# Kernel optimization log

Hardware: AMD Instinct MI355X
Metric: run time of the kernel (lower is better)

Reference implementation:

```python
import jax, jax.numpy as jnp
import numpy as np

NUM_HEADS = 16
HEAD_DIM = 96          # dim=1536 / 16 heads
ROPE_HALF = HEAD_DIM // 2   # 48 rotary frequencies
FREQ_PER_AXIS = ROPE_HALF // 3  # 16 frequencies per 3D coordinate axis
ROPE_BASE = 10000.0


def _rope_sincos(coords):
    # coords: [B, T, 3] -> sin, cos: [B, T, ROPE_HALF]
    inv_freq = 1.0 / (ROPE_BASE ** (jnp.arange(FREQ_PER_AXIS, dtype=jnp.float32) / FREQ_PER_AXIS))
    # angles per axis: [B, T, 3, F] -> concat axes -> [B, T, 3*F]
    ang = coords[..., :, None] * inv_freq  # [B, T, 3, F]
    ang = ang.reshape(*coords.shape[:-1], ROPE_HALF)
    return jnp.sin(ang), jnp.cos(ang)


def _apply_rotary(x, sin, cos):
    # x: [B, H, T, D]; sin/cos: [B, T, D/2] broadcast over heads
    s = sin[:, None, :, :]
    c = cos[:, None, :, :]
    x1, x2 = x[..., :ROPE_HALF], x[..., ROPE_HALF:]
    return jnp.concatenate([x1 * c - x2 * s, x2 * c + x1 * s], axis=-1)


def setup_inputs() -> dict:
    key = jax.random.key(0)
    ks = jax.random.split(key, 8)
    B, Tq, Tk, D = 2, 1024, 2048, 1536
    std = 1.0 / np.sqrt(D)
    return {
        "x": jax.random.normal(ks[0], (B, Tq, D), jnp.float32),
        "memory": jax.random.normal(ks[1], (B, Tk, D), jnp.float32),
        "query_coords": jax.random.normal(ks[2], (B, Tq, 3), jnp.float32),
        "memory_coords": jax.random.normal(ks[3], (B, Tk, 3), jnp.float32),
        "Wq": jax.random.normal(ks[4], (D, D), jnp.float32) * std,
        "bq": jnp.zeros((D,), jnp.float32),
        "Wk": jax.random.normal(ks[5], (D, D), jnp.float32) * std,
        "bk": jnp.zeros((D,), jnp.float32),
        "Wv": jax.random.normal(ks[6], (D, D), jnp.float32) * std,
        "bv": jnp.zeros((D,), jnp.float32),
        "Wo": jax.random.normal(ks[7], (D, D), jnp.float32) * std,
        "bo": jnp.zeros((D,), jnp.float32),
    }


def reference(x, memory, query_coords, memory_coords, Wq, bq, Wk, bk, Wv, bv, Wo, bo):
    B, Tq, D = x.shape
    Tk = memory.shape[1]
    H, Hd = NUM_HEADS, HEAD_DIM

    # projections (nn.Linear: y = x @ W^T + b)
    q = (jnp.einsum('btd,ed->bte', x, Wq) + bq).reshape(B, Tq, H, Hd).transpose(0, 2, 1, 3)
    k = (jnp.einsum('btd,ed->bte', memory, Wk) + bk).reshape(B, Tk, H, Hd).transpose(0, 2, 1, 3)
    v = (jnp.einsum('btd,ed->bte', memory, Wv) + bv).reshape(B, Tk, H, Hd).transpose(0, 2, 1, 3)

    # 3D-coordinate RoPE (identity augmentation: shift=0, jitter=1, rescale=1)
    q_sin, q_cos = _rope_sincos(query_coords)
    k_sin, k_cos = _rope_sincos(memory_coords)
    q = _apply_rotary(q, q_sin, q_cos)
    k = _apply_rotary(k, k_sin, k_cos)

    # SDPA (standard scaling): softmax(q k^T / sqrt(Hd)) v
    scale = 1.0 / jnp.sqrt(jnp.asarray(Hd, jnp.float32))
    scores = jnp.einsum('bhqd,bhkd->bhqk', q, k) * scale
    attn = jax.nn.softmax(scores, axis=-1)
    out = jnp.einsum('bhqk,bhkd->bhqd', attn, v)  # [B, H, Tq, Hd]

    out = out.transpose(0, 2, 1, 3).reshape(B, Tq, D)
    return jnp.einsum('btd,ed->bte', out, Wo) + bo
```

## Files before the change

### kernel.cpp

```cpp
#include <hip/hip_runtime.h>
#include <math.h>

typedef _Float16 f16;
typedef __attribute__((ext_vector_type(4))) _Float16 f16x4;
typedef __attribute__((ext_vector_type(8))) _Float16 f16x8;
typedef __attribute__((ext_vector_type(4))) float f32x4;
typedef __attribute__((ext_vector_type(16))) float f32x16;

#define NB 2
#define NH 16
#define TQ 1024
#define TK 2048
#define DM 1536
#define HD 96
#define RH 48

__device__ __forceinline__ f32x4 mfma16(f16x8 a, f16x8 b, f32x4 c) {
    return __builtin_amdgcn_mfma_f32_16x16x32_f16(a, b, c, 0, 0, 0);
}

#define GLDS16(gptr, lptr) __builtin_amdgcn_global_load_lds( \
    (const __attribute__((address_space(1))) unsigned int*)(gptr), \
    (__attribute__((address_space(3))) unsigned int*)(lptr), 16, 0, 0)

__global__ void cvt6(const float4* __restrict__ Wq, const float4* __restrict__ Wk,
                     const float4* __restrict__ Wv, const float4* __restrict__ Wo,
                     const float4* __restrict__ X,  const float4* __restrict__ M,
                     f16x4* __restrict__ oq, f16x4* __restrict__ ok,
                     f16x4* __restrict__ ov, f16x4* __restrict__ oo,
                     f16x4* __restrict__ ox, f16x4* __restrict__ om,
                     int nw4, int nx4, int nm4) {
    int i = blockIdx.x * 256 + threadIdx.x;
    const int y = blockIdx.y;
    const int n = (y < 4) ? nw4 : (y == 4 ? nx4 : nm4);
    if (i >= n) return;
    const float4* in = y == 0 ? Wq : y == 1 ? Wk : y == 2 ? Wv : y == 3 ? Wo : y == 4 ? X : M;
    f16x4* out      = y == 0 ? oq : y == 1 ? ok : y == 2 ? ov : y == 3 ? oo : y == 4 ? ox : om;
    float4 v = in[i];
    f16x4 o;
    o[0] = (f16)v.x; o[1] = (f16)v.y; o[2] = (f16)v.z; o[3] = (f16)v.w;
    out[i] = o;
}

__global__ void rope_tab2(const float* __restrict__ cq, const float* __restrict__ cm,
                          float* __restrict__ sq, float* __restrict__ cqo,
                          float* __restrict__ sk, float* __restrict__ cko,
                          int nq, int nk) {
    int i = blockIdx.x * 256 + threadIdx.x;
    int n = blockIdx.y == 0 ? nq : nk;
    if (i >= n) return;
    const float* coords = blockIdx.y == 0 ? cq : cm;
    float* sinT = blockIdx.y == 0 ? sq : sk;
    float* cosT = blockIdx.y == 0 ? cqo : cko;
    int bt = i / 48, idx = i - bt * 48;
    int axis = idx >> 4, f = idx & 15;
    float inv = powf(10000.f, -(float)f * (1.f / 16.f));
    float ang = coords[bt * 3 + axis] * inv;
    sinT[i] = sinf(ang);
    cosT[i] = cosf(ang);
}

__global__ void ropek4(f16* __restrict__ qk, const float* __restrict__ sinT,
                       const float* __restrict__ cosT, int n) {
    int i = blockIdx.x * 256 + threadIdx.x;
    if (i >= n) return;
    int j = i % 12, row = i / 12;
    int p0 = j * 4;
    int t = row & (TK - 1);
    int b = row / (NH * TK);
    long base = (long)row * 128;
    float4 sv = *(const float4*)&sinT[((long)b * TK + t) * 48 + p0];
    float4 cv = *(const float4*)&cosT[((long)b * TK + t) * 48 + p0];
    f16x4 x1 = *(const f16x4*)&qk[base + p0];
    f16x4 x2 = *(const f16x4*)&qk[base + p0 + RH];
    f16x4 o1, o2;
    float s[4] = {sv.x, sv.y, sv.z, sv.w}, c[4] = {cv.x, cv.y, cv.z, cv.w};
#pragma unroll
    for (int e = 0; e < 4; e++) {
        float a = (float)x1[e], bb = (float)x2[e];
        o1[e] = (f16)(a * c[e] - bb * s[e]);
        o2[e] = (f16)(bb * c[e] + a * s[e]);
    }
    *(f16x4*)&qk[base + p0] = o1;
    *(f16x4*)&qk[base + p0 + RH] = o2;
}

template <int CFG>
__global__ __launch_bounds__(CFG == 0 ? 512 : 256, CFG == 0 ? 1 : 2)
void gemmP(const f16* __restrict__ Aq, const f16* __restrict__ Akv,
           const f16* __restrict__ Wqp, const f16* __restrict__ Wkp, const f16* __restrict__ Wvp,
           const float* __restrict__ bqp, const float* __restrict__ bkp, const float* __restrict__ bvp,
           f16* __restrict__ outq, f16* __restrict__ outk, f16* __restrict__ outv,
           float* __restrict__ outo) {
    constexpr int BMx = CFG == 0 ? 256 : 128;
    constexpr int BNx = CFG == 0 ? 256 : 128;
    constexpr int TPB = CFG == 0 ? 512 : 256;
    constexpr int MI  = CFG == 0 ? 8 : 4;
    constexpr int NI  = 4;
    constexpr int ABUF = BMx * 64;
    constexpr int BUFSZ = (BMx + BNx) * 64;
    constexpr int NT = DM / 64;

    __shared__ f16 Buf[2][BUFSZ];

    const int tid = threadIdx.x, w = tid >> 6, lane = tid & 63;
    const int l15 = lane & 15, g = lane >> 4;

    int sel = 0, mt, nt;
    const f16* A; const f16* W; const float* bias;
    if constexpr (CFG == 0) {
        const int bid = blockIdx.x;
        const int wid = (bid & 7) * 30 + (bid >> 3);
        if (wid < 48)       { sel = 0; mt = wid / 6;        nt = wid - mt * 6;        A = Aq;  W = Wqp; bias = bqp; }
        else if (wid < 144) { sel = 1; int r = wid - 48;  mt = r / 6; nt = r - mt * 6; A = Akv; W = Wkp; bias = bkp; }
        else                { sel = 2; int r = wid - 144; mt = r / 6; nt = r - mt * 6; A = Akv; W = Wvp; bias = bvp; }
    } else {
        const int bid = blockIdx.x;
        const int wid = (bid & 7) * 24 + (bid >> 3);
        mt = wid / 12; nt = wid - mt * 12;
        A = Aq; W = Wqp; bias = bqp;
    }
    const int m0 = mt * BMx, n0 = nt * BNx;
    const int wm = (w & 1) * (MI * 16);
    const int wn = (w >> 1) * 64;

    int src[4];
#pragma unroll
    for (int r = 0; r < 4; r++) {
        int L = r * (TPB * 16) + tid * 16;
        int row = L >> 7, seg = (L >> 4) & 7;
        src[r] = row * DM + ((seg ^ (row & 7)) << 3);
    }
    const f16* Ag = A + (long)m0 * DM;
    const f16* Bg = W + (long)n0 * DM;

    int aoff[MI][2], boff[NI][2];
#pragma unroll
    for (int i = 0; i < MI; i++) {
        int row = wm + i * 16 + l15;
#pragma unroll
        for (int s = 0; s < 2; s++)
            aoff[i][s] = row * 64 + (((s * 4 + g) ^ (row & 7)) << 3);
    }
#pragma unroll
    for (int j = 0; j < NI; j++) {
        int row = wn + j * 16 + l15;
#pragma unroll
        for (int s = 0; s < 2; s++)
            boff[j][s] = ABUF + row * 64 + (((s * 4 + g) ^ (row & 7)) << 3);
    }

#define STG(bufp, kt) do { \
    _Pragma("unroll") for (int r_ = 0; r_ < 4; r_++) { \
        GLDS16(Ag + src[r_] + (kt) * 64, &Buf[bufp][r_ * (TPB * 8) + w * 512]); \
        GLDS16(Bg + src[r_] + (kt) * 64, &Buf[bufp][ABUF + r_ * (TPB * 8) + w * 512]); \
    } \
} while (0)

    f32x4 acc[MI][NI] = {};

#define COMPUTE(bufp) do { \
    f16x8 bf[NI][2]; \
    _Pragma("unroll") for (int j_ = 0; j_ < NI; j_++) \
        _Pragma("unroll") for (int s_ = 0; s_ < 2; s_++) \
            bf[j_][s_] = *(const f16x8*)&Buf[bufp][boff[j_][s_]]; \
    __builtin_amdgcn_s_setprio(1); \
    _Pragma("unroll") for (int i_ = 0; i_ < MI; i_++) { \
        f16x8 a0 = *(const f16x8*)&Buf[bufp][aoff[i_][0]]; \
        f16x8 a1 = *(const f16x8*)&Buf[bufp][aoff[i_][1]]; \
        _Pragma("unroll") for (int j_ = 0; j_ < NI; j_++) { \
            acc[i_][j_] = mfma16(a0, bf[j_][0], acc[i_][j_]); \
            acc[i_][j_] = mfma16(a1, bf[j_][1], acc[i_][j_]); \
        } \
    } \
    __builtin_amdgcn_s_setprio(0); \
} while (0)

    STG(0, 0);
#pragma unroll 1
    for (int t = 0; t < NT; t += 2) {
        STG(1, t + 1);
        asm volatile("s_waitcnt vmcnt(8)" ::: "memory");
        __builtin_amdgcn_s_barrier();
        __builtin_amdgcn_sched_barrier(0);
        COMPUTE(0);
        __builtin_amdgcn_sched_barrier(0);
        __builtin_amdgcn_s_barrier();
        if (t + 2 < NT) {
            STG(0, t + 2);
            asm volatile("s_waitcnt vmcnt(8)" ::: "memory");
        } else {
            asm volatile("s_waitcnt vmcnt(0)" ::: "memory");
        }
        __builtin_amdgcn_s_barrier();
        __builtin_amdgcn_sched_barrier(0);
        COMPUTE(1);
        __builtin_amdgcn_sched_barrier(0);
        __builtin_amdgcn_s_barrier();
    }
#undef STG
#undef COMPUTE

#pragma unroll
    for (int i = 0; i < MI; i++) {
#pragma unroll
        for (int j = 0; j < NI; j++) {
            const int n = n0 + wn + j * 16 + l15;
            const int mb = m0 + wm + i * 16 + g * 4;
            if constexpr (CFG == 1) {
#pragma unroll
                for (int r = 0; r < 4; r++)
                    outo[(long)(mb + r) * DM + n] = acc[i][j][r] + bias[n];
            } else {
                const int hh = n / HD, hd = n - hh * HD;
                if (sel == 0) {
#pragma unroll
                    for (int r = 0; r < 4; r++) {
                        int m = mb + r, bq = m >> 10, t = m & (TQ - 1);
                        outq[(((long)bq * NH + hh) * TQ + t) * 96 + hd] = (f16)(acc[i][j][r] + bias[n]);
                    }
                } else if (sel == 1) {
#pragma unroll
                    for (int r = 0; r < 4; r++) {
                        int m = mb + r, bq = m >> 11, t = m & (TK - 1);
                        outk[(((long)bq * NH + hh) * TK + t) * 128 + hd] = (f16)(acc[i][j][r] + bias[n]);
                    }
                } else {
                    int bq = mb >> 11, t = mb & (TK - 1);
                    f16x4 pk;
#pragma unroll
                    for (int r = 0; r < 4; r++) pk[r] = (f16)(acc[i][j][r] + bias[n]);
                    *(f16x4*)&outv[(((long)bq * NH + hh) * HD + hd) * TK + t] = pk;
                }
            }
        }
    }
}

__global__ __launch_bounds__(256, 2) void attn_fwd(
    const f16* __restrict__ Q, const f16* __restrict__ Kg,
    const f16* __restrict__ Vg, const float* __restrict__ sinq,
    const float* __restrict__ cosq, f16* __restrict__ O) {
    __shared__ f16 Kl[2][64 * 128];
    __shared__ f16 Vl[2][96 * 64];
    __shared__ f16 Pl[4][32 * 64];

    const int tid = threadIdx.x, w = tid >> 6, lane = tid & 63;
    const int q31 = lane & 31, hf = lane >> 5;
    const int half = w >> 1, u = w & 1;

    const int linear = blockIdx.x + (int)(gridDim.x * (blockIdx.y + gridDim.y * blockIdx.z));
    const int wid = (linear & 7) * 64 + (linear >> 3);
    const int qc = wid & 15, h = (wid >> 4) & 15, b = wid >> 8;

    const long kbase = (long)(b * NH + h) * TK * 128;
    const long vbase = (long)(b * NH + h) * HD * TK;
    const long qbase = (long)(b * NH + h) * TQ * 96;
    const int q0 = qc * 64 + u * 32;

    int ksrc[8], vsrc[6];
#pragma unroll
    for (int i = 0; i < 8; i++) {
        int L = (u * 8 + i) * 1024 + lane * 16;
        int r = L >> 8, s = (L >> 4) & 15;
        ksrc[i] = r * 128 + ((s ^ (r & 7)) << 3);
    }
#pragma unroll
    for (int i = 0; i < 6; i++) {
        int L = (u * 6 + i) * 1024 + lane * 16;
        int r = L >> 7, s = (L >> 4) & 7;
        vsrc[i] = r * TK + ((s ^ (r & 7)) << 3);
    }

    f16x8 qf[6];
#pragma unroll
    for (int s = 0; s < 6; s++)
        qf[s] = *(const f16x8*)&Q[qbase + (long)(q0 + q31) * 96 + hf * 8 + 16 * s];
    {
        const float QS = 0.10206207261596577f * 1.4426950408889634f;
        const long tb = ((long)b * TQ + q0 + q31) * 48 + hf * 8;
#pragma unroll
        for (int s = 0; s < 3; s++) {
            float4 s0 = *(const float4*)&sinq[tb + 16 * s];
            float4 s1 = *(const float4*)&sinq[tb + 16 * s + 4];
            float4 c0 = *(const float4*)&cosq[tb + 16 * s];
            float4 c1 = *(const float4*)&cosq[tb + 16 * s + 4];
            float sv[8] = {s0.x, s0.y, s0.z, s0.w, s1.x, s1.y, s1.z, s1.w};
            float cv[8] = {c0.x, c0.y, c0.z, c0.w, c1.x, c1.y, c1.z, c1.w};
#pragma unroll
            for (int e = 0; e < 8; e++) {
                float x1 = (float)qf[s][e], x2 = (float)qf[s + 3][e];
                qf[s][e]     = (f16)((x1 * cv[e] - x2 * sv[e]) * QS);
                qf[s + 3][e] = (f16)((x2 * cv[e] + x1 * sv[e]) * QS);
            }
        }
    }

    float mx = -3e38f, ls = 0.f;
    f32x16 acc[3] = {};

#define STAGE(c_) do { \
    const f16* kp_ = Kg + kbase + (long)(half * 16 + (c_)) * (64 * 128); \
    _Pragma("unroll") for (int i_ = 0; i_ < 8; i_++) \
        GLDS16(kp_ + ksrc[i_], &Kl[half][(u * 8 + i_) * 512]); \
    const f16* vp_ = Vg + vbase + (half * 16 + (c_)) * 64; \
    _Pragma("unroll") for (int i_ = 0; i_ < 6; i_++) \
        GLDS16(vp_ + vsrc[i_], &Vl[half][(u * 6 + i_) * 512]); \
} while (0)

    STAGE(0);

    for (int c = 0; c < 16; ++c) {
        __syncthreads();

        f32x16 st[2] = {};
#pragma unroll
        for (int kt = 0; kt < 2; kt++)
#pragma unroll
            for (int s = 0; s < 6; s++) {
                f16x8 kf = *(const f16x8*)&Kl[half][(kt * 32 + q31) * 128 +
                                                    (((hf + 2 * s) ^ (q31 & 7)) << 3)];
                st[kt] = __builtin_amdgcn_mfma_f32_32x32x16_f16(kf, qf[s], st[kt], 0, 0, 0);
            }

        float t16[16];
#pragma unroll
        for (int r = 0; r < 16; r++) t16[r] = fmaxf(st[0][r], st[1][r]);
#pragma unroll
        for (int o = 8; o >= 1; o >>= 1)
#pragma unroll
            for (int r = 0; r < o; r++) t16[r] = fmaxf(t16[r], t16[r + o]);
        float cm = fmaxf(t16[0], __shfl_xor(t16[0], 32));
        float mn = fmaxf(mx, cm);
        float corr = exp2f(mx - mn);
        mx = mn;
#pragma unroll
        for (int kt = 0; kt < 2; kt++)
#pragma unroll
            for (int r = 0; r < 16; r++) st[kt][r] = exp2f(st[kt][r] - mn);
        float s16[16];
#pragma unroll
        for (int r = 0; r < 16; r++) s16[r] = st[0][r] + st[1][r];
#pragma unroll
        for (int o = 8; o >= 1; o >>= 1)
#pragma unroll
            for (int r = 0; r < o; r++) s16[r] += s16[r + o];
        ls = ls * corr + s16[0];
#pragma unroll
        for (int dt = 0; dt < 3; dt++)
#pragma unroll
            for (int r = 0; r < 16; r++) acc[dt][r] *= corr;

#pragma unroll
        for (int kt = 0; kt < 2; kt++)
#pragma unroll
            for (int jq = 0; jq < 4; jq++) {
                f16x4 pk;
#pragma unroll
                for (int e = 0; e < 4; e++) pk[e] = (f16)st[kt][jq * 4 + e];
                int seg = kt * 4 + jq;
                *(f16x4*)&Pl[w][q31 * 64 + ((seg ^ (q31 & 7)) << 3) + hf * 4] = pk;
            }

#pragma unroll
        for (int ks = 0; ks < 4; ks++) {
            f16x8 pf = *(const f16x8*)&Pl[w][q31 * 64 + (((hf + 2 * ks) ^ (q31 & 7)) << 3)];
#pragma unroll
            for (int dt = 0; dt < 3; dt++) {
                f16x8 vf = *(const f16x8*)&Vl[half][(dt * 32 + q31) * 64 +
                                                    (((hf + 2 * ks) ^ (q31 & 7)) << 3)];
                acc[dt] = __builtin_amdgcn_mfma_f32_32x32x16_f16(vf, pf, acc[dt], 0, 0, 0);
            }
        }

        __syncthreads();
        if (c < 15) STAGE(c + 1);
    }

    ls += __shfl_xor(ls, 32);
    float* dump = (float*)&Kl[0][0] + u * (64 * 52);
    __syncthreads();
    if (half == 1) {
        float* dl = dump + lane * 52;
        dl[0] = mx; dl[1] = ls;
#pragma unroll
        for (int dt = 0; dt < 3; dt++)
#pragma unroll
            for (int r = 0; r < 16; r++) dl[2 + dt * 16 + r] = acc[dt][r];
    }
    __syncthreads();
    if (half == 0) {
        const float* dl = dump + lane * 52;
        float mb = dl[0], lsb = dl[1];
        float mf = fmaxf(mx, mb);
        float ca = exp2f(mx - mf), cb = exp2f(mb - mf);
        float inv = 1.f / (ls * ca + lsb * cb);
        const long orow = (long)(b * TQ + q0 + q31) * DM + h * 96;
#pragma unroll
        for (int dt = 0; dt < 3; dt++)
#pragma unroll
            for (int jq = 0; jq < 4; jq++) {
                f16x4 ov;
#pragma unroll
                for (int e = 0; e < 4; e++) {
                    int r = jq * 4 + e;
                    ov[e] = (f16)((acc[dt][r] * ca + dl[2 + dt * 16 + r] * cb) * inv);
                }
                *(f16x4*)&O[orow + dt * 32 + jq * 8 + hf * 4] = ov;
            }
    }
}

extern "C" void kernel_launch(void* const* d_in, const int* in_sizes, int n_in,
                              void* d_out, int out_size, void* d_ws, size_t ws_size,
                              hipStream_t stream) {
    const float* x   = (const float*)d_in[0];
    const float* mem = (const float*)d_in[1];
    const float* qc  = (const float*)d_in[2];
    const float* mc  = (const float*)d_in[3];
    const float* Wq  = (const float*)d_in[4];
    const float* bq  = (const float*)d_in[5];
    const float* Wk  = (const float*)d_in[6];
    const float* bk  = (const float*)d_in[7];
    const float* Wv  = (const float*)d_in[8];
    const float* bv  = (const float*)d_in[9];
    const float* Wo  = (const float*)d_in[10];
    const float* bo  = (const float*)d_in[11];
    float* out = (float*)d_out;

    const long nx  = (long)NB * TQ * DM;
    const long nm  = (long)NB * TK * DM;
    const long nw  = (long)DM * DM;
    const long nq  = (long)NB * NH * TQ * 96;
    const long nkp = (long)NB * NH * TK * 128;
    const long nvt = (long)NB * NH * HD * TK;

    char* ws = (char*)d_ws;
    size_t off = 0;
    auto alloc = [&](size_t bytes) { size_t o = off; off = (off + bytes + 255) & ~(size_t)255; return o; };
    f16* x16   = (f16*)(ws + alloc(nx * 2));
    f16* mem16 = (f16*)(ws + alloc(nm * 2));
    f16* wq16  = (f16*)(ws + alloc(nw * 2));
    f16* wk16  = (f16*)(ws + alloc(nw * 2));
    f16* wv16  = (f16*)(ws + alloc(nw * 2));
    f16* wo16  = (f16*)(ws + alloc(nw * 2));
    f16* q16   = (f16*)(ws + alloc(nq * 2));
    f16* k16p  = (f16*)(ws + alloc(nkp * 2));
    f16* vt16  = (f16*)(ws + alloc(nvt * 2));
    float* sinq = (float*)(ws + alloc((size_t)NB * TQ * 48 * 4));
    float* cosq = (float*)(ws + alloc((size_t)NB * TQ * 48 * 4));
    float* sink = (float*)(ws + alloc((size_t)NB * TK * 48 * 4));
    float* cosk = (float*)(ws + alloc((size_t)NB * TK * 48 * 4));
    f16* at16 = x16;

    cvt6<<<dim3((int)(nm / 4 / 256), 6), 256, 0, stream>>>(
        (const float4*)Wq, (const float4*)Wk, (const float4*)Wv, (const float4*)Wo,
        (const float4*)x, (const float4*)mem,
        (f16x4*)wq16, (f16x4*)wk16, (f16x4*)wv16, (f16x4*)wo16,
        (f16x4*)x16, (f16x4*)mem16,
        (int)(nw / 4), (int)(nx / 4), (int)(nm / 4));

    rope_tab2<<<dim3((NB * TK * 48 + 255) / 256, 2), 256, 0, stream>>>(
        qc, mc, sinq, cosq, sink, cosk, NB * TQ * 48, NB * TK * 48);

    gemmP<0><<<240, 512, 0, stream>>>(
        x16, mem16, wq16, wk16, wv16, bq, bk, bv, q16, k16p, vt16, nullptr);

    ropek4<<<(NB * NH * TK * 12 + 255) / 256, 256, 0, stream>>>(
        k16p, sink, cosk, NB * NH * TK * 12);

    attn_fwd<<<dim3(16, 16, 2), 256, 0, stream>>>(q16, k16p, vt16, sinq, cosq, at16);

    gemmP<1><<<192, 256, 0, stream>>>(
        at16, nullptr, wo16, nullptr, nullptr, bo, nullptr, nullptr,
        nullptr, nullptr, nullptr, out);
}
```

Before: 155.8 us.

## Load QKV GEMM weight tiles directly into registers instead of LDS

The templated GEMM is split into a dedicated QKV kernel and an output-projection kernel. In the QKV kernel, the B (weight) operand fragments are now loaded from global memory straight into registers, double-buffered, and only the A tile is staged through LDS. This halves LDS usage and LDS read traffic per tile, at the cost of more vector registers and uncoalesced, non-shared global loads of weights across waves. The O-projection kernel keeps the previous scheme.

```diff
diff --git a/kernel.cpp b/kernel.cpp
--- a/kernel.cpp
+++ b/kernel.cpp
@@ -85,43 +85,163 @@
     *(f16x4*)&qk[base + p0 + RH] = o2;
 }
 
-template <int CFG>
-__global__ __launch_bounds__(CFG == 0 ? 512 : 256, CFG == 0 ? 1 : 2)
-void gemmP(const f16* __restrict__ Aq, const f16* __restrict__ Akv,
-           const f16* __restrict__ Wqp, const f16* __restrict__ Wkp, const f16* __restrict__ Wvp,
-           const float* __restrict__ bqp, const float* __restrict__ bkp, const float* __restrict__ bvp,
-           f16* __restrict__ outq, f16* __restrict__ outk, f16* __restrict__ outv,
-           float* __restrict__ outo) {
-    constexpr int BMx = CFG == 0 ? 256 : 128;
-    constexpr int BNx = CFG == 0 ? 256 : 128;
-    constexpr int TPB = CFG == 0 ? 512 : 256;
-    constexpr int MI  = CFG == 0 ? 8 : 4;
-    constexpr int NI  = 4;
-    constexpr int ABUF = BMx * 64;
-    constexpr int BUFSZ = (BMx + BNx) * 64;
+__global__ __launch_bounds__(512, 1)
+void gemmQKV(const f16* __restrict__ Aq, const f16* __restrict__ Akv,
+             const f16* __restrict__ Wqp, const f16* __restrict__ Wkp, const f16* __restrict__ Wvp,
+             const float* __restrict__ bqp, const float* __restrict__ bkp, const float* __restrict__ bvp,
+             f16* __restrict__ outq, f16* __restrict__ outk, f16* __restrict__ outv) {
+    constexpr int MI = 8, NI = 4;
     constexpr int NT = DM / 64;
 
-    __shared__ f16 Buf[2][BUFSZ];
+    __shared__ f16 Buf[2][256 * 64];
 
     const int tid = threadIdx.x, w = tid >> 6, lane = tid & 63;
     const int l15 = lane & 15, g = lane >> 4;
 
     int sel = 0, mt, nt;
     const f16* A; const f16* W; const float* bias;
-    if constexpr (CFG == 0) {
+    {
         const int bid = blockIdx.x;
         const int wid = (bid & 7) * 30 + (bid >> 3);
         if (wid < 48)       { sel = 0; mt = wid / 6;        nt = wid - mt * 6;        A = Aq;  W = Wqp; bias = bqp; }
         else if (wid < 144) { sel = 1; int r = wid - 48;  mt = r / 6; nt = r - mt * 6; A = Akv; W = Wkp; bias = bkp; }
         else                { sel = 2; int r = wid - 144; mt = r / 6; nt = r - mt * 6; A = Akv; W = Wvp; bias = bvp; }
-    } else {
-        const int bid = blockIdx.x;
-        const int wid = (bid & 7) * 24 + (bid >> 3);
-        mt = wid / 12; nt = wid - mt * 12;
-        A = Aq; W = Wqp; bias = bqp;
-    }
-    const int m0 = mt * BMx, n0 = nt * BNx;
-    const int wm = (w & 1) * (MI * 16);
+    }
+    const int m0 = mt * 256, n0 = nt * 256;
+    const int wm = (w & 1) * 128;
+    const int wn = (w >> 1) * 64;
+
+    int src[4];
+#pragma unroll
+    for (int r = 0; r < 4; r++) {
+        int L = r * 8192 + tid * 16;
+        int row = L >> 7, seg = (L >> 4) & 7;
+        src[r] = row * DM + ((seg ^ (row & 7)) << 3);
+    }
+    const f16* Ag = A + (long)m0 * DM;
+
+    int aoff[MI][2];
+#pragma unroll
+    for (int i = 0; i < MI; i++) {
+        int row = wm + i * 16 + l15;
+#pragma unroll
+        for (int s = 0; s < 2; s++)
+            aoff[i][s] = row * 64 + (((s * 4 + g) ^ (row & 7)) << 3);
+    }
+
+    const f16* bptr[NI];
+#pragma unroll
+    for (int j = 0; j < NI; j++)
+        bptr[j] = W + (long)(n0 + wn + j * 16 + l15) * DM + g * 8;
+
+#define STG(bufp, kt) do { \
+    _Pragma("unroll") for (int r_ = 0; r_ < 4; r_++) \
+        GLDS16(Ag + src[r_] + (kt) * 64, &Buf[bufp][r_ * 4096 + w * 512]); \
+} while (0)
+
+#define LDB(breg, kt) do { \
+    _Pragma("unroll") for (int j_ = 0; j_ < NI; j_++) \
+        _Pragma("unroll") for (int s_ = 0; s_ < 2; s_++) \
+            breg[j_][s_] = *(const f16x8*)(bptr[j_] + (kt) * 64 + s_ * 32); \
+} while (0)
+
+    f32x4 acc[MI][NI] = {};
+
+#define COMPUTE(bufp, breg) do { \
+    __builtin_amdgcn_s_setprio(1); \
+    _Pragma("unroll") for (int i_ = 0; i_ < MI; i_++) { \
+        f16x8 a0 = *(const f16x8*)&Buf[bufp][aoff[i_][0]]; \
+        f16x8 a1 = *(const f16x8*)&Buf[bufp][aoff[i_][1]]; \
+        _Pragma("unroll") for (int j_ = 0; j_ < NI; j_++) { \
+            acc[i_][j_] = mfma16(a0, breg[j_][0], acc[i_][j_]); \
+            acc[i_][j_] = mfma16(a1, breg[j_][1], acc[i_][j_]); \
+        } \
+    } \
+    __builtin_amdgcn_s_setprio(0); \
+} while (0)
+
+    f16x8 bA[NI][2], bB[NI][2];
+    STG(0, 0);
+    LDB(bA, 0);
+
+#pragma unroll 1
+    for (int t = 0; t < NT; t += 2) {
+        if (t + 1 < NT) {
+            STG(1, t + 1);
+            LDB(bB, t + 1);
+            asm volatile("s_waitcnt vmcnt(12)" ::: "memory");
+        } else {
+            asm volatile("s_waitcnt vmcnt(0)" ::: "memory");
+        }
+        __builtin_amdgcn_s_barrier();
+        __builtin_amdgcn_sched_barrier(0);
+        COMPUTE(0, bA);
+        __builtin_amdgcn_sched_barrier(0);
+        __builtin_amdgcn_s_barrier();
+        if (t + 2 < NT) {
+            STG(0, t + 2);
+            LDB(bA, t + 2);
+            asm volatile("s_waitcnt vmcnt(12)" ::: "memory");
+        } else {
+            asm volatile("s_waitcnt vmcnt(0)" ::: "memory");
+        }
+        __builtin_amdgcn_s_barrier();
+        __builtin_amdgcn_sched_barrier(0);
+        COMPUTE(1, bB);
+        __builtin_amdgcn_sched_barrier(0);
+        __builtin_amdgcn_s_barrier();
+    }
+#undef STG
+#undef LDB
+#undef COMPUTE
+
+#pragma unroll
+    for (int i = 0; i < MI; i++) {
+#pragma unroll
+        for (int j = 0; j < NI; j++) {
+            const int n = n0 + wn + j * 16 + l15;
+            const int mb = m0 + wm + i * 16 + g * 4;
+            const int hh = n / HD, hd = n - hh * HD;
+            if (sel == 0) {
+#pragma unroll
+                for (int r = 0; r < 4; r++) {
+                    int m = mb + r, bq = m >> 10, t = m & (TQ - 1);
+                    outq[(((long)bq * NH + hh) * TQ + t) * 96 + hd] = (f16)(acc[i][j][r] + bias[n]);
+                }
+            } else if (sel == 1) {
+#pragma unroll
+                for (int r = 0; r < 4; r++) {
+                    int m = mb + r, bq = m >> 11, t = m & (TK - 1);
+                    outk[(((long)bq * NH + hh) * TK + t) * 128 + hd] = (f16)(acc[i][j][r] + bias[n]);
+                }
+            } else {
+                int bq = mb >> 11, t = mb & (TK - 1);
+                f16x4 pk;
+#pragma unroll
+                for (int r = 0; r < 4; r++) pk[r] = (f16)(acc[i][j][r] + bias[n]);
+                *(f16x4*)&outv[(((long)bq * NH + hh) * HD + hd) * TK + t] = pk;
+            }
+        }
+    }
+}
+
+__global__ __launch_bounds__(256, 2)
+void gemmO(const f16* __restrict__ A, const f16* __restrict__ W,
+           const float* __restrict__ bias, float* __restrict__ outo) {
+    constexpr int TPB = 256, MI = 4, NI = 4;
+    constexpr int ABUF = 128 * 64;
+    constexpr int BUFSZ = 256 * 64;
+    constexpr int NT = DM / 64;
+
+    __shared__ f16 Buf[2][BUFSZ];
+
+    const int tid = threadIdx.x, w = tid >> 6, lane = tid & 63;
+    const int l15 = lane & 15, g = lane >> 4;
+    const int bid = blockIdx.x;
+    const int wid = (bid & 7) * 24 + (bid >> 3);
+    const int mt = wid / 12, nt = wid - mt * 12;
+    const int m0 = mt * 128, n0 = nt * 128;
+    const int wm = (w & 1) * 64;
     const int wn = (w >> 1) * 64;
 
     int src[4];
@@ -207,32 +327,9 @@
         for (int j = 0; j < NI; j++) {
             const int n = n0 + wn + j * 16 + l15;
             const int mb = m0 + wm + i * 16 + g * 4;
-            if constexpr (CFG == 1) {
-#pragma unroll
-                for (int r = 0; r < 4; r++)
-                    outo[(long)(mb + r) * DM + n] = acc[i][j][r] + bias[n];
-            } else {
-                const int hh = n / HD, hd = n - hh * HD;
-                if (sel == 0) {
-#pragma unroll
-                    for (int r = 0; r < 4; r++) {
-                        int m = mb + r, bq = m >> 10, t = m & (TQ - 1);
-                        outq[(((long)bq * NH + hh) * TQ + t) * 96 + hd] = (f16)(acc[i][j][r] + bias[n]);
-                    }
-                } else if (sel == 1) {
-#pragma unroll
-                    for (int r = 0; r < 4; r++) {
-                        int m = mb + r, bq = m >> 11, t = m & (TK - 1);
-                        outk[(((long)bq * NH + hh) * TK + t) * 128 + hd] = (f16)(acc[i][j][r] + bias[n]);
-                    }
-                } else {
-                    int bq = mb >> 11, t = mb & (TK - 1);
-                    f16x4 pk;
-#pragma unroll
-                    for (int r = 0; r < 4; r++) pk[r] = (f16)(acc[i][j][r] + bias[n]);
-                    *(f16x4*)&outv[(((long)bq * NH + hh) * HD + hd) * TK + t] = pk;
-                }
-            }
+#pragma unroll
+            for (int r = 0; r < 4; r++)
+                outo[(long)(mb + r) * DM + n] = acc[i][j][r] + bias[n];
         }
     }
 }
@@ -463,15 +560,13 @@
     rope_tab2<<<dim3((NB * TK * 48 + 255) / 256, 2), 256, 0, stream>>>(
         qc, mc, sinq, cosq, sink, cosk, NB * TQ * 48, NB * TK * 48);
 
-    gemmP<0><<<240, 512, 0, stream>>>(
-        x16, mem16, wq16, wk16, wv16, bq, bk, bv, q16, k16p, vt16, nullptr);
+    gemmQKV<<<240, 512, 0, stream>>>(
+        x16, mem16, wq16, wk16, wv16, bq, bk, bv, q16, k16p, vt16);
 
     ropek4<<<(NB * NH * TK * 12 + 255) / 256, 256, 0, stream>>>(
         k16p, sink, cosk, NB * NH * TK * 12);
 
     attn_fwd<<<dim3(16, 16, 2), 256, 0, stream>>>(q16, k16p, vt16, sinq, cosq, at16);
 
-    gemmP<1><<<192, 256, 0, stream>>>(
-        at16, nullptr, wo16, nullptr, nullptr, bo, nullptr, nullptr,
-        nullptr, nullptr, nullptr, out);
-}
+    gemmO<<<192, 256, 0, stream>>>(at16, wo16, bo, out);
+}
```

After: 177.7 us. 14.0% more time.
